# Optimization experiments

Hardware: AMD Instinct MI355X
Metric: run time of the kernel (lower is better)

The kernel has to match this reference:

```python
import jax, jax.numpy as jnp
import numpy as np

B, N, E, D, H, C, U = 512, 256, 1024, 256, 256, 8, 64
MARGIN_T, RISK_T, SCALE = 0.2, 0.6, 0.1
NEG = -1.0e9


def setup_inputs() -> dict:
    key = jax.random.key(0)
    ks = jax.random.split(key, 30)
    s = 0.02
    inp = dict(
        features=jax.random.normal(ks[0], (B, D), jnp.float32),
        centered_scores=jax.random.normal(ks[1], (B, N), jnp.float32),
        margin=jax.random.uniform(ks[2], (B,), jnp.float32),
        boundary_risk=jax.random.uniform(ks[3], (B,), jnp.float32),
        edge_sensitivity=jax.random.normal(ks[4], (B, E), jnp.float32),
        coords=jax.random.normal(ks[5], (B, N, C), jnp.float32),
        uncertainty=jax.random.uniform(ks[6], (B, U), jnp.float32),
        Wc1=jax.random.normal(ks[7], (D, H), jnp.float32) * s,
        bc1=jnp.zeros((H,), jnp.float32),
        Wc2=jax.random.normal(ks[8], (H, H), jnp.float32) * s,
        bc2=jnp.zeros((H,), jnp.float32),
        Wn1=jax.random.normal(ks[9], (H + C + 2, H), jnp.float32) * s,
        bn1=jnp.zeros((H,), jnp.float32),
        Wn2=jax.random.normal(ks[10], (H, 1), jnp.float32) * s,
        bn2=jnp.zeros((1,), jnp.float32),
        We1=jax.random.normal(ks[11], (H + C + 2, H), jnp.float32) * s,
        be1=jnp.zeros((H,), jnp.float32),
        We2=jax.random.normal(ks[12], (H, 1), jnp.float32) * s,
        be2=jnp.zeros((1,), jnp.float32),
        Wg=jax.random.normal(ks[13], (H, 1), jnp.float32) * s,
        bg=jnp.zeros((1,), jnp.float32),
        action_mask=jax.random.bernoulli(ks[14], 0.8, (B, N)),
        edge_mask=jax.random.bernoulli(ks[15], 0.8, (B, E)),
        actions=jax.random.randint(ks[16], (B, N), 0, U, jnp.int32),
        edges=jax.random.randint(ks[17], (B, E, 2), 0, N, jnp.int32),
    )
    return inp


def _mlp2(x, W1, b1, W2, b2):
    return jax.nn.relu(x @ W1 + b1) @ W2 + b2


def reference(features, centered_scores, margin, boundary_risk, edge_sensitivity,
              coords, uncertainty, Wc1, bc1, Wc2, bc2, Wn1, bn1, Wn2, bn2,
              We1, be1, We2, be2, Wg, bg, action_mask, edge_mask, actions, edges):
    amf = action_mask.astype(jnp.float32)
    emf = edge_mask.astype(jnp.float32)

    # context MLP
    h = jax.nn.relu(jax.nn.relu(features @ Wc1 + bc1) @ Wc2 + bc2)  # [B,H]

    low_margin = (margin < MARGIN_T).astype(jnp.float32)
    high_risk = (boundary_risk > RISK_T).astype(jnp.float32)
    learned_gate = jax.nn.sigmoid((h @ Wg + bg)[:, 0])
    refine_gate = jnp.maximum(jnp.maximum(low_margin, high_risk),
                              (learned_gate > 0.5).astype(jnp.float32))  # [B]

    # node features: [B,N,H+C+2]
    act = jnp.clip(actions, 0, U - 1)
    unc_g = jnp.take_along_axis(uncertainty, act, axis=1)  # [B,N]
    h_n = jnp.broadcast_to(h[:, None, :], (B, N, H))
    node_feats = jnp.concatenate(
        [h_n, coords, centered_scores[..., None], unc_g[..., None]], axis=-1)
    node_delta = _mlp2(node_feats, Wn1, bn1, Wn2, bn2)[..., 0] * amf  # [B,N]

    # edge features: gather src/dst coords
    e = jnp.clip(edges, 0, N - 1)
    src_c = jnp.take_along_axis(coords, e[:, :, 0:1], axis=1)  # [B,E,C]
    dst_c = jnp.take_along_axis(coords, e[:, :, 1:2], axis=1)  # [B,E,C]
    h_e = jnp.broadcast_to(h[:, None, :], (B, E, H))
    edge_feats = jnp.concatenate(
        [h_e, dst_c - src_c, edge_sensitivity[..., None], emf[..., None]], axis=-1)
    edge_delta = _mlp2(edge_feats, We1, be1, We2, be2)[..., 0] * emf  # [B,E]

    gate_node = refine_gate[:, None]
    refined_scores = (centered_scores + gate_node * SCALE * node_delta) * amf
    denom = jnp.clip(amf.sum(-1, keepdims=True), 1.0, None)  # [B,1]
    refined_scores = (refined_scores - refined_scores.sum(-1, keepdims=True) / denom) * amf

    refined_edge = (edge_sensitivity + gate_node * SCALE * edge_delta) * emf

    masked_top = jnp.where(action_mask, refined_scores, NEG)
    top_vals, top_idx = jax.lax.top_k(masked_top, 2)
    refined_margin = top_vals[:, 0] - top_vals[:, 1]

    # masked per-batch variance of refined_edge (biased), 0 if <=1 valid entry
    cnt = emf.sum(-1)
    cnt_c = jnp.clip(cnt, 1.0, None)
    mean = (refined_edge * emf).sum(-1) / cnt_c
    var = (emf * (refined_edge - mean[:, None]) ** 2).sum(-1) / cnt_c
    edge_var = jnp.where(cnt > 1.0, var, 0.0)

    unc_term = (unc_g * amf).sum(-1) / denom[:, 0]
    refined_risk = jnp.clip(
        jax.nn.sigmoid(-refined_margin) + 0.2 * edge_var + 0.1 * unc_term, 0.0, 1.0)

    return (refined_scores, refined_margin, refined_edge,
            top_idx[:, 0], refined_risk, refine_gate)
```

## Files before the change

### kernel.cpp

```cpp
#include <hip/hip_runtime.h>
#include <math.h>

#define B 512
#define N 256
#define E 1024
#define D 256
#define H 256
#define C 8
#define U 64

typedef __fp16 h2 __attribute__((ext_vector_type(2)));
union UF { float f; h2 h; unsigned u; };

__device__ __forceinline__ float bc_f(h2 h) { UF u; u.h = h; return u.f; }
__device__ __forceinline__ h2 bc_h(float f) { UF u; u.f = f; return u.h; }

#if __has_builtin(__builtin_amdgcn_cvt_pkrtz)
__device__ __forceinline__ h2 pkh(float a, float b) { return __builtin_amdgcn_cvt_pkrtz(a, b); }
#else
__device__ __forceinline__ h2 pkh(float a, float b) { h2 r; r.x = (__fp16)a; r.y = (__fp16)b; return r; }
#endif

#if __has_builtin(__builtin_amdgcn_fdot2)
__device__ __forceinline__ float FDOT2(h2 a, h2 b, float c) { return __builtin_amdgcn_fdot2(a, b, c, false); }
#else
__device__ __forceinline__ float FDOT2(h2 a, h2 b, float c) {
    return fmaf((float)a.x, (float)b.x, fmaf((float)a.y, (float)b.y, c));
}
#endif

__device__ __forceinline__ float mask_val(const void* m, long i, int flag) {
    if (flag == 1) return ((const unsigned char*)m)[i] ? 1.f : 0.f;
    if (flag == 2) return (((const float*)m)[i] != 0.f) ? 1.f : 0.f;
    return ((const int*)m)[i] ? 1.f : 0.f;
}

__device__ __forceinline__ float block_sum(float v, float* red) {
    int t = threadIdx.x;
    red[t] = v; __syncthreads();
    for (int s = 128; s > 0; s >>= 1) {
        if (t < s) red[t] += red[t + s];
        __syncthreads();
    }
    float r = red[0]; __syncthreads();
    return r;
}

__global__ __launch_bounds__(512) void k_h(
    const float* __restrict__ feat,
    const float* __restrict__ Wc1, const float* __restrict__ bc1,
    const float* __restrict__ Wc2, const float* __restrict__ bc2,
    const float* __restrict__ Wn1, const float* __restrict__ bn1,
    const float* __restrict__ We1, const float* __restrict__ be1,
    const float* __restrict__ Wg,  const float* __restrict__ bg,
    const float* __restrict__ margin, const float* __restrict__ brisk,
    const unsigned int* __restrict__ amask_words,
    float* __restrict__ base_n, float* __restrict__ base_e,
    float* __restrict__ out_gate, int* __restrict__ flag,
    float* __restrict__ node_delta, float* __restrict__ out2)
{
    __shared__ __align__(16) float sF[2][256];
    __shared__ __align__(16) float sH[2][256];
    __shared__ float red[512];
    __shared__ int cls0, cls1;

    int t = threadIdx.x;
    int w = t >> 8;
    int c = t & 255;
    int b0 = blockIdx.x * 2;
    int b = b0 + w;

    {
        int idx = blockIdx.x * 512 + t;
        node_delta[idx] = 0.f;
        ((float4*)out2)[idx] = make_float4(0.f, 0.f, 0.f, 0.f);
    }

    if (blockIdx.x == 0) {
        if (t == 0) { cls0 = 0; cls1 = 0; }
        __syncthreads();
        if (t < 256) {
            unsigned int wd = amask_words[t];
            if (wd != 0u && wd != 1u) {
                if (wd == 0x3f800000u) atomicOr(&cls1, 1);
                else                   atomicOr(&cls0, 1);
            }
        }
        __syncthreads();
        if (t == 0) *flag = cls0 ? 1 : (cls1 ? 2 : 0);
    }

    sF[w][c] = feat[(long)b * D + c];
    __syncthreads();

    {
        float acc[4] = {bc1[c], 0.f, 0.f, 0.f};
        const float* Wp = Wc1 + c;
        for (int d0 = 0; d0 < D; d0 += 16) {
            float wv[16];
            #pragma unroll
            for (int k = 0; k < 16; k++) wv[k] = Wp[(long)(d0 + k) * H];
            #pragma unroll
            for (int k = 0; k < 16; k++)
                acc[k & 3] = fmaf(sF[w][d0 + k], wv[k], acc[k & 3]);
        }
        sH[w][c] = fmaxf((acc[0] + acc[1]) + (acc[2] + acc[3]), 0.f);
    }
    __syncthreads();

    {
        float acc[4] = {bc2[c], 0.f, 0.f, 0.f};
        const float* Wp = Wc2 + c;
        for (int d0 = 0; d0 < H; d0 += 16) {
            float wv[16];
            #pragma unroll
            for (int k = 0; k < 16; k++) wv[k] = Wp[(long)(d0 + k) * H];
            #pragma unroll
            for (int k = 0; k < 16; k++)
                acc[k & 3] = fmaf(sH[w][d0 + k], wv[k], acc[k & 3]);
        }
        float a = fmaxf((acc[0] + acc[1]) + (acc[2] + acc[3]), 0.f);
        __syncthreads();
        sF[w][c] = a;
    }
    __syncthreads();

    red[t] = sF[w][c] * Wg[c];
    __syncthreads();
    for (int s = 128; s > 0; s >>= 1) {
        if (c < s) red[t] += red[t + s];
        __syncthreads();
    }
    if (c == 0) {
        float lg = 1.f / (1.f + expf(-(red[t] + bg[0])));
        out_gate[b] = ((margin[b] < 0.2f) || (brisk[b] > 0.6f) || (lg > 0.5f)) ? 1.f : 0.f;
    }

    {
        const float* W3  = w ? (We1 + c) : (Wn1 + c);
        float bias       = w ? be1[c]    : bn1[c];
        float* dst       = w ? base_e    : base_n;
        float aA[2] = {bias, 0.f};
        float aB[2] = {bias, 0.f};
        for (int d0 = 0; d0 < H; d0 += 16) {
            float wv[16];
            #pragma unroll
            for (int k = 0; k < 16; k++) wv[k] = W3[(long)(d0 + k) * H];
            #pragma unroll
            for (int k = 0; k < 16; k++) {
                aA[k & 1] = fmaf(sF[0][d0 + k], wv[k], aA[k & 1]);
                aB[k & 1] = fmaf(sF[1][d0 + k], wv[k], aB[k & 1]);
            }
        }
        dst[(long)b0 * H + c]       = aA[0] + aA[1];
        dst[(long)(b0 + 1) * H + c] = aB[0] + aB[1];
    }
}

__global__ __launch_bounds__(256, 2) void k_ne(
    const float* __restrict__ cs, const float* __restrict__ coords,
    const float* __restrict__ unc, const int* __restrict__ actions,
    const float* __restrict__ Wn1, const float* __restrict__ Wn2,
    const float* __restrict__ base_n,
    const float* __restrict__ es, const int* __restrict__ edges,
    const float* __restrict__ We1, const float* __restrict__ We2,
    const float* __restrict__ base_e,
    const float* __restrict__ gate,
    float* __restrict__ node_delta, float* __restrict__ out2)
{
    __shared__ __align__(16) float smem[3840];
    int t = threadIdx.x;
    int w = t >> 6, lane = t & 63;

    if (blockIdx.x < 512) {
        int rg = blockIdx.x >> 2;
        int jq = blockIdx.x & 3;
        int b0 = rg * 4;
        float* pack = smem;
        float* sB   = smem + 768;

        {
            int i = t;
            #pragma unroll
            for (int s = 0; s < 3; s++, i += 256) {
                int j = i / 12, k = i - j * 12;
                int jj = jq * 64 + j;
                float v;
                if (k < 10)       v = Wn1[(long)(H + k) * H + jj];
                else if (k == 10) v = Wn2[jj];
                else              v = 0.f;
                pack[i] = v;
            }
            int r = t >> 6, j = t & 63;
            sB[r * 64 + j] = base_n[(long)(b0 + r) * H + jq * 64 + j];
        }
        __syncthreads();

        int b = b0 + w;
        float g = gate[b];
        if (g != 0.f) {
            float f8v[4], ug[4], acc[4];
            float f0[4], f1[4], f2[4], f3[4], f4[4], f5[4], f6[4], f7[4];
            #pragma unroll
            for (int q = 0; q < 4; q++) {
                int n = q * 64 + lane;
                const float4* cp = (const float4*)(coords + ((long)b * N + n) * C);
                float4 c0 = cp[0], c1 = cp[1];
                f0[q] = c0.x; f1[q] = c0.y; f2[q] = c0.z; f3[q] = c0.w;
                f4[q] = c1.x; f5[q] = c1.y; f6[q] = c1.z; f7[q] = c1.w;
                f8v[q] = cs[(long)b * N + n];
                int a = actions[(long)b * N + n];
                a = min(max(a, 0), U - 1);
                ug[q] = unc[(long)b * U + a];
                acc[q] = 0.f;
            }

            const float* sBw = sB + w * 64;
            #pragma unroll 4
            for (int j = 0; j < 64; j++) {
                const float* pj = pack + j * 12;
                float4 wa = *(const float4*)(pj);
                float4 wb = *(const float4*)(pj + 4);
                float4 wc = *(const float4*)(pj + 8);
                float bse = sBw[j];
                #pragma unroll
                for (int q = 0; q < 4; q++) {
                    float zA = fmaf(f0[q], wa.x, bse);
                    zA = fmaf(f1[q], wa.y, zA);
                    zA = fmaf(f2[q], wa.z, zA);
                    zA = fmaf(f3[q], wa.w, zA);
                    float zB = f4[q] * wb.x;
                    zB = fmaf(f5[q], wb.y, zB);
                    zB = fmaf(f6[q], wb.z, zB);
                    zB = fmaf(f7[q], wb.w, zB);
                    zB = fmaf(f8v[q], wc.x, zB);
                    zB = fmaf(ug[q], wc.y, zB);
                    acc[q] = fmaf(fmaxf(zA + zB, 0.f), wc.z, acc[q]);
                }
            }

            #pragma unroll
            for (int q = 0; q < 4; q++)
                atomicAdd(&node_delta[(long)b * N + q * 64 + lane], acc[q]);
        }
    } else {
        int eb = blockIdx.x - 512;
        int b = eb >> 2, jq = eb & 3;
        float g = gate[b];
        if (g == 0.f) return;

        float*  A4 = smem;
        float2* B2 = (float2*)(smem + 256);
        float*  sC = smem + 768;

        {
            const float4* g4 = (const float4*)(coords + (long)b * N * C);
            float4 c0 = g4[2 * t], c1 = g4[2 * t + 1];
            float4* d0 = (float4*)(sC + t * 12);
            d0[0] = c0; d0[1] = c1;
        }
        if (t < 64) {
            int j = jq * 64 + t;
            float w0 = We1[(long)(H + 0) * H + j];
            float w1 = We1[(long)(H + 1) * H + j];
            float w2 = We1[(long)(H + 2) * H + j];
            float w3 = We1[(long)(H + 3) * H + j];
            float w4 = We1[(long)(H + 4) * H + j];
            float w5 = We1[(long)(H + 5) * H + j];
            float w6 = We1[(long)(H + 6) * H + j];
            float w7 = We1[(long)(H + 7) * H + j];
            float w8 = We1[(long)(H + 8) * H + j];
            float w9 = We1[(long)(H + 9) * H + j];
            float we2 = We2[j];
            float bse = base_e[(long)b * H + j] + w9;
            float4 av;
            av.x = bc_f(pkh(w0, w1)); av.y = bc_f(pkh(w2, w3));
            av.z = bc_f(pkh(w4, w5)); av.w = bc_f(pkh(w6, w7));
            ((float4*)A4)[t] = av;
            B2[t] = make_float2(bc_f(pkh(w8, we2)), bse);
        }
        __syncthreads();

        float p01[4], p23[4], p45[4], p67[4], pes[4], acc[4];
        #pragma unroll
        for (int q = 0; q < 4; q++) {
            int e = w * 256 + q * 64 + lane;
            long idx = (long)b * E + e;
            int2 ev = ((const int2*)edges)[idx];
            int s0 = min(max(ev.x, 0), N - 1);
            int d0 = min(max(ev.y, 0), N - 1);
            const float4* cs4 = (const float4*)(sC + s0 * 12);
            const float4* cd4 = (const float4*)(sC + d0 * 12);
            float4 sa = cs4[0], sb = cs4[1];
            float4 da = cd4[0], db = cd4[1];
            p01[q] = bc_f(pkh(da.x - sa.x, da.y - sa.y));
            p23[q] = bc_f(pkh(da.z - sa.z, da.w - sa.w));
            p45[q] = bc_f(pkh(db.x - sb.x, db.y - sb.y));
            p67[q] = bc_f(pkh(db.z - sb.z, db.w - sb.w));
            pes[q] = bc_f(pkh(es[idx], 0.f));
            acc[q] = 0.f;
        }

        const float4* A4v = (const float4*)A4;
        #pragma unroll 4
        for (int j = 0; j < 64; j++) {
            float4 av = A4v[j];
            float2 bv = B2[j];
            h2 w01 = bc_h(av.x), w23 = bc_h(av.y);
            h2 w45 = bc_h(av.z), w67 = bc_h(av.w);
            h2 w8x = bc_h(bv.x);
            float we2f = (float)(w8x.y);
            float bse = bv.y;
            #pragma unroll
            for (int q = 0; q < 4; q++) {
                float z = FDOT2(bc_h(p01[q]), w01, bse);
                z = FDOT2(bc_h(p23[q]), w23, z);
                z = FDOT2(bc_h(p45[q]), w45, z);
                z = FDOT2(bc_h(p67[q]), w67, z);
                z = FDOT2(bc_h(pes[q]), w8x, z);
                acc[q] = fmaf(fmaxf(z, 0.f), we2f, acc[q]);
            }
        }

        #pragma unroll
        for (int q = 0; q < 4; q++)
            atomicAdd(&out2[(long)b * E + w * 256 + q * 64 + lane], acc[q]);
    }
}

__global__ __launch_bounds__(256) void k_fin(
    const void* __restrict__ amask, const void* __restrict__ emask,
    const int* __restrict__ actions, const float* __restrict__ unc,
    const float* __restrict__ cs, const float* __restrict__ es,
    const float* __restrict__ bn2, const float* __restrict__ be2,
    const float* __restrict__ gate, const int* __restrict__ flagp,
    const float* __restrict__ node_delta,
    float* __restrict__ out0, float* __restrict__ out1,
    float* __restrict__ out2, float* __restrict__ out3,
    float* __restrict__ riskbase, float* __restrict__ evar)
{
    __shared__ float red[256];
    __shared__ int ridx[256];
    int t = threadIdx.x;
    int flag = *flagp;

    if (blockIdx.x < B) {
        int b = blockIdx.x;
        float g = gate[b];
        float am = mask_val(amask, (long)b * N + t, flag);
        float csv = cs[(long)b * N + t];
        int a = actions[(long)b * N + t];
        a = min(max(a, 0), U - 1);
        float ug = unc[(long)b * U + a];
        float nd = (node_delta[(long)b * N + t] + bn2[0]) * am;
        float raw = (csv + g * 0.1f * nd) * am;

        float sum = block_sum(raw, red);
        float cnt = block_sum(am, red);
        float denom = fmaxf(cnt, 1.f);
        float rs = (raw - sum / denom) * am;
        out0[(long)b * N + t] = rs;

        float masked = (am != 0.f) ? rs : -1e9f;

        red[t] = masked; ridx[t] = t; __syncthreads();
        for (int s = 128; s > 0; s >>= 1) {
            if (t < s) {
                float o = red[t + s]; int oi = ridx[t + s];
                if (o > red[t] || (o == red[t] && oi < ridx[t])) { red[t] = o; ridx[t] = oi; }
            }
            __syncthreads();
        }
        float v1 = red[0]; int i1 = ridx[0]; __syncthreads();

        red[t] = (t == i1) ? -1e9f : masked; __syncthreads();
        for (int s = 128; s > 0; s >>= 1) {
            if (t < s) red[t] = fmaxf(red[t], red[t + s]);
            __syncthreads();
        }
        float v2 = red[0]; __syncthreads();
        float rmargin = v1 - v2;

        float su = block_sum(ug * am, red);

        if (t == 0) {
            out1[b] = rmargin;
            out3[b] = (float)i1;
            float sig = 1.f / (1.f + expf(rmargin));
            riskbase[b] = sig + 0.1f * (su / denom);
        }
    } else {
        int b = blockIdx.x - B;
        float g = gate[b];
        float be2v = be2[0];

        float re[4], emv[4];
        #pragma unroll
        for (int q = 0; q < 4; q++) {
            long idx = (long)b * E + t + 256 * q;
            emv[q] = mask_val(emask, idx, flag);
            float delta = out2[idx] + be2v;
            float r = es[idx] + g * 0.1f * delta;
            re[q] = (emv[q] != 0.f) ? r : 0.f;
            out2[idx] = re[q];
        }

        float S1 = 0.f, ce = 0.f;
        #pragma unroll
        for (int q = 0; q < 4; q++) { S1 += re[q]; ce += emv[q]; }
        float S1t = block_sum(S1, red);
        float cet = block_sum(ce, red);
        float mean = S1t / fmaxf(cet, 1.f);
        float v = 0.f;
        #pragma unroll
        for (int q = 0; q < 4; q++) {
            float dd = re[q] - mean;
            v = fmaf(emv[q] * dd, dd, v);
        }
        float vt = block_sum(v, red);
        if (t == 0) {
            float var = vt / fmaxf(cet, 1.f);
            evar[b] = (cet > 1.f) ? var : 0.f;
        }
    }
}

__global__ __launch_bounds__(256) void k_risk(
    const float* __restrict__ riskbase, const float* __restrict__ evar,
    float* __restrict__ out4)
{
    int b = blockIdx.x * 256 + threadIdx.x;
    float r = riskbase[b] + 0.2f * evar[b];
    out4[b] = fminf(fmaxf(r, 0.f), 1.f);
}

extern "C" void kernel_launch(void* const* d_in, const int* in_sizes, int n_in,
                              void* d_out, int out_size, void* d_ws, size_t ws_size,
                              hipStream_t stream) {
    const float* feat   = (const float*)d_in[0];
    const float* cs     = (const float*)d_in[1];
    const float* marg   = (const float*)d_in[2];
    const float* brisk  = (const float*)d_in[3];
    const float* es     = (const float*)d_in[4];
    const float* coords = (const float*)d_in[5];
    const float* unc    = (const float*)d_in[6];
    const float* Wc1    = (const float*)d_in[7];
    const float* bc1    = (const float*)d_in[8];
    const float* Wc2    = (const float*)d_in[9];
    const float* bc2    = (const float*)d_in[10];
    const float* Wn1    = (const float*)d_in[11];
    const float* bn1    = (const float*)d_in[12];
    const float* Wn2    = (const float*)d_in[13];
    const float* bn2    = (const float*)d_in[14];
    const float* We1    = (const float*)d_in[15];
    const float* be1    = (const float*)d_in[16];
    const float* We2    = (const float*)d_in[17];
    const float* be2    = (const float*)d_in[18];
    const float* Wg     = (const float*)d_in[19];
    const float* bg     = (const float*)d_in[20];
    const void*  amask  = d_in[21];
    const void*  emask  = d_in[22];
    const int*   actions= (const int*)d_in[23];
    const int*   edges  = (const int*)d_in[24];

    float* out0 = (float*)d_out;
    float* out1 = out0 + (long)B * N;
    float* out2 = out1 + B;
    float* out3 = out2 + (long)B * E;
    float* out4 = out3 + B;
    float* out5 = out4 + B;

    float* base_n     = (float*)d_ws;
    float* base_e     = base_n + (long)B * H;
    float* node_delta = base_e + (long)B * H;
    float* riskbase   = node_delta + (long)B * N;
    float* evar       = riskbase + B;
    int*   flag       = (int*)(evar + B);

    k_h<<<B / 2, 512, 0, stream>>>(feat, Wc1, bc1, Wc2, bc2, Wn1, bn1, We1, be1,
                                   Wg, bg, marg, brisk,
                                   (const unsigned int*)amask,
                                   base_n, base_e, out5, flag,
                                   node_delta, out2);
    k_ne<<<512 + 4 * B, 256, 0, stream>>>(cs, coords, unc, actions,
                                          Wn1, Wn2, base_n,
                                          es, edges,
                                          We1, We2, base_e,
                                          out5, node_delta, out2);
    k_fin<<<2 * B, 256, 0, stream>>>(amask, emask, actions, unc, cs, es,
                                     bn2, be2, out5, flag, node_delta,
                                     out0, out1, out2, out3, riskbase, evar);
    k_risk<<<2, 256, 0, stream>>>(riskbase, evar, out4);
}
```

Before: 72.28 us.

## Precompute packed fp16 edge coordinate deltas in first kernel for edge MLP

Result: slower. 74.83 us (+3.5%).

```diff
diff --git a/kernel.cpp b/kernel.cpp
--- a/kernel.cpp
+++ b/kernel.cpp
@@ -55,13 +55,17 @@
     const float* __restrict__ Wg,  const float* __restrict__ bg,
     const float* __restrict__ margin, const float* __restrict__ brisk,
     const unsigned int* __restrict__ amask_words,
+    const float* __restrict__ coords, const int* __restrict__ edges,
+    const float* __restrict__ es,
     float* __restrict__ base_n, float* __restrict__ base_e,
     float* __restrict__ out_gate, int* __restrict__ flag,
-    float* __restrict__ node_delta, float* __restrict__ out2)
+    float* __restrict__ node_delta, float* __restrict__ out2,
+    float* __restrict__ planes, int pre)
 {
     __shared__ __align__(16) float sF[2][256];
     __shared__ __align__(16) float sH[2][256];
     __shared__ float red[512];
+    __shared__ __align__(16) float sC[2][3072];
     __shared__ int cls0, cls1;
 
     int t = threadIdx.x;
@@ -88,6 +92,41 @@
         }
         __syncthreads();
         if (t == 0) *flag = cls0 ? 1 : (cls1 ? 2 : 0);
+    }
+
+    if (pre) {
+        float* plane0 = planes;
+        float* plane1 = planes + (long)B * E;
+        float* plane2 = planes + 2L * B * E;
+        float* plane3 = planes + 3L * B * E;
+        float* plane4 = planes + 4L * B * E;
+
+        int rr = w, nn = c;
+        int brow = b0 + rr;
+        {
+            const float4* cp = (const float4*)(coords + ((long)brow * N + nn) * C);
+            float4 c0 = cp[0], c1 = cp[1];
+            float* dst = sC[rr] + nn * 12;
+            dst[0] = c0.x; dst[1] = c0.y; dst[2] = c0.z; dst[3] = c0.w;
+            dst[4] = c1.x; dst[5] = c1.y; dst[6] = c1.z; dst[7] = c1.w;
+        }
+        __syncthreads();
+        #pragma unroll
+        for (int k = 0; k < 4; k++) {
+            int e = k * 256 + nn;
+            long idx = (long)brow * E + e;
+            int2 ev = ((const int2*)edges)[idx];
+            int s0 = min(max(ev.x, 0), N - 1);
+            int d0 = min(max(ev.y, 0), N - 1);
+            const float* cs0 = sC[rr] + s0 * 12;
+            const float* cd0 = sC[rr] + d0 * 12;
+            plane0[idx] = bc_f(pkh(cd0[0] - cs0[0], cd0[1] - cs0[1]));
+            plane1[idx] = bc_f(pkh(cd0[2] - cs0[2], cd0[3] - cs0[3]));
+            plane2[idx] = bc_f(pkh(cd0[4] - cs0[4], cd0[5] - cs0[5]));
+            plane3[idx] = bc_f(pkh(cd0[6] - cs0[6], cd0[7] - cs0[7]));
+            plane4[idx] = bc_f(pkh(es[idx], 0.f));
+        }
+        __syncthreads();
     }
 
     sF[w][c] = feat[(long)b * D + c];
@@ -166,7 +205,8 @@
     const float* __restrict__ We1, const float* __restrict__ We2,
     const float* __restrict__ base_e,
     const float* __restrict__ gate,
-    float* __restrict__ node_delta, float* __restrict__ out2)
+    float* __restrict__ node_delta, float* __restrict__ out2,
+    const float* __restrict__ planes, int pre)
 {
     __shared__ __align__(16) float smem[3840];
     int t = threadIdx.x;
@@ -253,12 +293,6 @@
         float2* B2 = (float2*)(smem + 256);
         float*  sC = smem + 768;
 
-        {
-            const float4* g4 = (const float4*)(coords + (long)b * N * C);
-            float4 c0 = g4[2 * t], c1 = g4[2 * t + 1];
-            float4* d0 = (float4*)(sC + t * 12);
-            d0[0] = c0; d0[1] = c1;
-        }
         if (t < 64) {
             int j = jq * 64 + t;
             float w0 = We1[(long)(H + 0) * H + j];
@@ -279,26 +313,50 @@
             ((float4*)A4)[t] = av;
             B2[t] = make_float2(bc_f(pkh(w8, we2)), bse);
         }
-        __syncthreads();
 
         float p01[4], p23[4], p45[4], p67[4], pes[4], acc[4];
-        #pragma unroll
-        for (int q = 0; q < 4; q++) {
-            int e = w * 256 + q * 64 + lane;
-            long idx = (long)b * E + e;
-            int2 ev = ((const int2*)edges)[idx];
-            int s0 = min(max(ev.x, 0), N - 1);
-            int d0 = min(max(ev.y, 0), N - 1);
-            const float4* cs4 = (const float4*)(sC + s0 * 12);
-            const float4* cd4 = (const float4*)(sC + d0 * 12);
-            float4 sa = cs4[0], sb = cs4[1];
-            float4 da = cd4[0], db = cd4[1];
-            p01[q] = bc_f(pkh(da.x - sa.x, da.y - sa.y));
-            p23[q] = bc_f(pkh(da.z - sa.z, da.w - sa.w));
-            p45[q] = bc_f(pkh(db.x - sb.x, db.y - sb.y));
-            p67[q] = bc_f(pkh(db.z - sb.z, db.w - sb.w));
-            pes[q] = bc_f(pkh(es[idx], 0.f));
-            acc[q] = 0.f;
+        if (pre) {
+            const float* plane0 = planes;
+            const float* plane1 = planes + (long)B * E;
+            const float* plane2 = planes + 2L * B * E;
+            const float* plane3 = planes + 3L * B * E;
+            const float* plane4 = planes + 4L * B * E;
+            __syncthreads();
+            #pragma unroll
+            for (int q = 0; q < 4; q++) {
+                long idx = (long)b * E + w * 256 + q * 64 + lane;
+                p01[q] = plane0[idx];
+                p23[q] = plane1[idx];
+                p45[q] = plane2[idx];
+                p67[q] = plane3[idx];
+                pes[q] = plane4[idx];
+                acc[q] = 0.f;
+            }
+        } else {
+            {
+                const float4* g4 = (const float4*)(coords + (long)b * N * C);
+                float4 c0 = g4[2 * t], c1 = g4[2 * t + 1];
+                float4* d0 = (float4*)(sC + t * 12);
+                d0[0] = c0; d0[1] = c1;
+            }
+            __syncthreads();
+            #pragma unroll
+            for (int q = 0; q < 4; q++) {
+                long idx = (long)b * E + w * 256 + q * 64 + lane;
+                int2 ev = ((const int2*)edges)[idx];
+                int s0 = min(max(ev.x, 0), N - 1);
+                int d0 = min(max(ev.y, 0), N - 1);
+                const float4* cs4 = (const float4*)(sC + s0 * 12);
+                const float4* cd4 = (const float4*)(sC + d0 * 12);
+                float4 sa = cs4[0], sb = cs4[1];
+                float4 da = cd4[0], db = cd4[1];
+                p01[q] = bc_f(pkh(da.x - sa.x, da.y - sa.y));
+                p23[q] = bc_f(pkh(da.z - sa.z, da.w - sa.w));
+                p45[q] = bc_f(pkh(db.x - sb.x, db.y - sb.y));
+                p67[q] = bc_f(pkh(db.z - sb.z, db.w - sb.w));
+                pes[q] = bc_f(pkh(es[idx], 0.f));
+                acc[q] = 0.f;
+            }
         }
 
         const float4* A4v = (const float4*)A4;
@@ -476,17 +534,23 @@
     float* riskbase   = node_delta + (long)B * N;
     float* evar       = riskbase + B;
     int*   flag       = (int*)(evar + B);
+    float* planes     = (float*)(flag + 16);
+
+    size_t fixed_bytes = (size_t)((char*)planes - (char*)d_ws);
+    size_t plane_bytes = 5L * B * E * sizeof(float);
+    int pre = (ws_size >= fixed_bytes + plane_bytes) ? 1 : 0;
 
     k_h<<<B / 2, 512, 0, stream>>>(feat, Wc1, bc1, Wc2, bc2, Wn1, bn1, We1, be1,
                                    Wg, bg, marg, brisk,
                                    (const unsigned int*)amask,
+                                   coords, edges, es,
                                    base_n, base_e, out5, flag,
-                                   node_delta, out2);
+                                   node_delta, out2, planes, pre);
     k_ne<<<512 + 4 * B, 256, 0, stream>>>(cs, coords, unc, actions,
                                           Wn1, Wn2, base_n,
                                           es, edges,
                                           We1, We2, base_e,
-                                          out5, node_delta, out2);
+                                          out5, node_delta, out2, planes, pre);
     k_fin<<<2 * B, 256, 0, stream>>>(amask, emask, actions, unc, cs, es,
                                      bn2, be2, out5, flag, node_delta,
                                      out0, out1, out2, out3, riskbase, evar);
```
